# Optimization experiments

Hardware: AMD Instinct MI355X
Metric: run time of the kernel (lower is better)

## Reference

```python
import jax, jax.numpy as jnp
from jax import lax
import numpy as np

D_MODEL = 1024
N_HEADS = 16
D_STATE = D_MODEL // N_HEADS  # 64
EPS = 1e-6


def setup_inputs() -> dict:
    key = jax.random.key(0)
    ks = jax.random.split(key, 8)
    B, S = 4, 4096
    s = 1.0 / np.sqrt(D_MODEL)
    return {
        "x": jax.random.normal(ks[0], (B, S, D_MODEL), dtype=jnp.float32),
        "state": jnp.zeros((B, N_HEADS, D_STATE), dtype=jnp.float32),
        "norm_w": jnp.ones((D_MODEL,), dtype=jnp.float32),
        "Wp": jax.random.normal(ks[1], (D_MODEL, 3 * N_HEADS * D_STATE), dtype=jnp.float32) * s,
        "bp": jax.random.normal(ks[2], (3 * N_HEADS * D_STATE,), dtype=jnp.float32) * 0.01,
        "Wg": jax.random.normal(ks[3], (D_MODEL, D_MODEL), dtype=jnp.float32) * s,
        "bg": jax.random.normal(ks[4], (D_MODEL,), dtype=jnp.float32) * 0.01,
        "Wo": jax.random.normal(ks[5], (D_MODEL, D_MODEL), dtype=jnp.float32) * s,
        "bo": jax.random.normal(ks[6], (D_MODEL,), dtype=jnp.float32) * 0.01,
    }


def reference(x, state, norm_w, Wp, bp, Wg, bg, Wo, bo):
    B, S, D = x.shape
    # RMSNorm
    rms = jnp.sqrt(jnp.mean(x * x, axis=-1, keepdims=True) + EPS)
    xn = norm_w * x / rms
    # input-dependent gate and SSM parameters (all per-timestep, vectorized)
    gate = jax.nn.sigmoid(xn @ Wg + bg)                        # (B,S,D)
    p = (xn @ Wp + bp).reshape(B, S, N_HEADS, 3, D_STATE)
    delta = jax.nn.sigmoid(p[..., 0, :])                       # (B,S,H,Ds)
    Bt = p[..., 1, :]
    Ct = p[..., 2, :]
    # sequential recurrence h_{t+1} = delta_t * h_t + B_t via lax.scan over time
    def step(h, db):
        d, b = db
        h = d * h + b
        return h, h
    dT = jnp.moveaxis(delta, 1, 0)  # (S,B,H,Ds)
    bT = jnp.moveaxis(Bt, 1, 0)
    new_state, hs = lax.scan(step, state, (dT, bT))
    hs = jnp.moveaxis(hs, 0, 1)     # (B,S,H,Ds)
    ssm = (Ct * hs).reshape(B, S, D)
    mixed = gate * ssm + (1.0 - gate) * xn
    y = mixed @ Wo + bo + x         # out_proj + residual (dropout=0)
    return y, new_state
```

## Files before the change

### kernel.cpp

```cpp
#include <hip/hip_runtime.h>
#include <hip/hip_bf16.h>
#include <cstdint>
#include <cstddef>

#define D_MODEL 1024
#define N_HEADS 16
#define D_STATE 64
#define SEQ 4096
#define BATCH 4
#define M_TOK (BATCH * SEQ)
#define N1 4096
#define CLEN 128
#define NCH (SEQ / CLEN)
#define NCHAN (BATCH * D_MODEL)

typedef __attribute__((ext_vector_type(8))) short bf16x8;
typedef __attribute__((ext_vector_type(4))) float f32x4;

__device__ __forceinline__ float sigmoidf_(float x) {
    return 1.0f / (1.0f + __expf(-x));
}

__device__ __forceinline__ void async_load16(const void* g, void* l) {
    __builtin_amdgcn_global_load_lds(
        (__attribute__((address_space(1))) void*)(g),
        (__attribute__((address_space(3))) void*)(l), 16, 0, 0);
}

__global__ __launch_bounds__(256) void transpose_cvt(
    const float* __restrict__ src, __hip_bfloat16* __restrict__ dst,
    int K, int N)
{
    __shared__ float tile[32][33];
    int n0 = blockIdx.x * 32, k0 = blockIdx.y * 32;
    int tx = threadIdx.x, ty = threadIdx.y;
#pragma unroll
    for (int j = 0; j < 32; j += 8)
        tile[ty + j][tx] = src[(size_t)(k0 + ty + j) * N + n0 + tx];
    __syncthreads();
#pragma unroll
    for (int j = 0; j < 32; j += 8)
        dst[(size_t)(n0 + ty + j) * K + k0 + tx] = __float2bfloat16(tile[tx][ty + j]);
}

__global__ __launch_bounds__(256) void rmsnorm_kernel(
    const float* __restrict__ x, const float* __restrict__ w,
    __hip_bfloat16* __restrict__ xn)
{
    int m = blockIdx.x;
    int tid = threadIdx.x;
    const float4* xr = (const float4*)(x + (size_t)m * D_MODEL);
    float4 v = xr[tid];
    float ss = v.x * v.x + v.y * v.y + v.z * v.z + v.w * v.w;
#pragma unroll
    for (int o = 32; o >= 1; o >>= 1) ss += __shfl_xor(ss, o, 64);
    __shared__ float red[4];
    int wave = tid >> 6, lane = tid & 63;
    if (lane == 0) red[wave] = ss;
    __syncthreads();
    float tot = red[0] + red[1] + red[2] + red[3];
    float scale = rsqrtf(tot * (1.0f / D_MODEL) + 1e-6f);
    const float4* wr = (const float4*)w;
    float4 wv = wr[tid];
    __hip_bfloat16 o4[4];
    o4[0] = __float2bfloat16(wv.x * v.x * scale);
    o4[1] = __float2bfloat16(wv.y * v.y * scale);
    o4[2] = __float2bfloat16(wv.z * v.z * scale);
    o4[3] = __float2bfloat16(wv.w * v.w * scale);
    *(uint64_t*)(xn + (size_t)m * D_MODEL + tid * 4) = *(uint64_t*)o4;
}


__device__ __forceinline__ void stage8(const short*& Ag, const short*& Bg,
                                       short* dbase, int stL, int K)
{
    short* la = dbase;
    short* lb = dbase + 16384;
#pragma unroll
    for (int l = 0; l < 4; ++l) {
        async_load16(Ag + (size_t)(l * 64) * K, la + stL + l * 4096);
        async_load16(Bg + (size_t)(l * 64) * K, lb + stL + l * 4096);
    }
    Ag += 64;
    Bg += 64;
}

template <int MODE>
__global__ __launch_bounds__(512, 2) void gemm256(
    const __hip_bfloat16* __restrict__ A,
    const __hip_bfloat16* __restrict__ Bt,
    const float* __restrict__ bias0,
    const float* __restrict__ bias1,
    void* __restrict__ outp, int N, int K)
{
    extern __shared__ short lds[];
    const int tid = threadIdx.x;
    const int wave = tid >> 6, lane = tid & 63;
    const int fr = lane & 15, fq = lane >> 4;
    const int frx = fr & 7;
    const int wm = (wave >> 2) * 128;
    const int wn = (wave & 3) * 64;

    const int gx = gridDim.x;
    const int nwg = gx * gridDim.y;
    const int orig = blockIdx.y * gx + blockIdx.x;
    const int swz = (orig & 7) * (nwg >> 3) + (orig >> 3);
    const int m0 = (swz / gx) * 256;
    const int n0 = (swz % gx) * 256;

    const int rb = tid >> 3, p8 = tid & 7;
    const int lsl = p8 ^ (rb & 7);
    const short* Ag = (const short*)A + (size_t)(m0 + rb) * K + lsl * 8;
    const short* Bg = (const short*)Bt + (size_t)(n0 + rb) * K + lsl * 8;
    const int stL = rb * 64 + p8 * 8;

    const int NT = K >> 6;

    f32x4 acc[2][4][4];
#pragma unroll
    for (int h = 0; h < 2; ++h)
#pragma unroll
        for (int i = 0; i < 4; ++i)
#pragma unroll
            for (int j = 0; j < 4; ++j)
                acc[h][i][j] = (f32x4){0.f, 0.f, 0.f, 0.f};

    stage8(Ag, Bg, lds, stL, K);
    stage8(Ag, Bg, lds + 32768, stL, K);

#define LDA(h, i, kk) (*(const bf16x8*)&Ab[(wm + (h)*64 + (i)*16 + fr) * 64 + \
                                           (((kk)*4 + fq) ^ frx) * 8])
#define LDB(j, kk)    (*(const bf16x8*)&Bb[(wn + (j)*16 + fr) * 64 + \
                                           (((kk)*4 + fq) ^ frx) * 8])

    for (int kt = 0; kt < NT; ++kt) {
        if (kt + 1 < NT) { asm volatile("s_waitcnt vmcnt(8)" ::: "memory"); }
        else             { asm volatile("s_waitcnt vmcnt(0)" ::: "memory"); }
        __builtin_amdgcn_s_barrier();
        __builtin_amdgcn_sched_barrier(0);

        const short* Ab = lds + ((kt & 1) ? 32768 : 0);
        const short* Bb = Ab + 16384;

        bf16x8 af[4][2], b0[2][2], b1[2][2];

#pragma unroll
        for (int i = 0; i < 4; ++i) { af[i][0] = LDA(0, i, 0); af[i][1] = LDA(0, i, 1); }
#pragma unroll
        for (int j = 0; j < 2; ++j) { b0[j][0] = LDB(j, 0); b0[j][1] = LDB(j, 1); }
        __builtin_amdgcn_s_setprio(1);
#pragma unroll
        for (int i = 0; i < 4; ++i)
#pragma unroll
            for (int j = 0; j < 2; ++j) {
                acc[0][i][j] = __builtin_amdgcn_mfma_f32_16x16x32_bf16(af[i][0], b0[j][0], acc[0][i][j], 0, 0, 0);
                acc[0][i][j] = __builtin_amdgcn_mfma_f32_16x16x32_bf16(af[i][1], b0[j][1], acc[0][i][j], 0, 0, 0);
            }
        __builtin_amdgcn_s_setprio(0);
        __builtin_amdgcn_sched_barrier(0);

#pragma unroll
        for (int j = 0; j < 2; ++j) { b1[j][0] = LDB(2 + j, 0); b1[j][1] = LDB(2 + j, 1); }
        __builtin_amdgcn_s_setprio(1);
#pragma unroll
        for (int i = 0; i < 4; ++i)
#pragma unroll
            for (int j = 0; j < 2; ++j) {
                acc[0][i][2 + j] = __builtin_amdgcn_mfma_f32_16x16x32_bf16(af[i][0], b1[j][0], acc[0][i][2 + j], 0, 0, 0);
                acc[0][i][2 + j] = __builtin_amdgcn_mfma_f32_16x16x32_bf16(af[i][1], b1[j][1], acc[0][i][2 + j], 0, 0, 0);
            }
        __builtin_amdgcn_s_setprio(0);
        __builtin_amdgcn_sched_barrier(0);

#pragma unroll
        for (int i = 0; i < 4; ++i) { af[i][0] = LDA(1, i, 0); af[i][1] = LDA(1, i, 1); }
        __builtin_amdgcn_s_setprio(1);
#pragma unroll
        for (int i = 0; i < 4; ++i)
#pragma unroll
            for (int j = 0; j < 2; ++j) {
                acc[1][i][j] = __builtin_amdgcn_mfma_f32_16x16x32_bf16(af[i][0], b0[j][0], acc[1][i][j], 0, 0, 0);
                acc[1][i][j] = __builtin_amdgcn_mfma_f32_16x16x32_bf16(af[i][1], b0[j][1], acc[1][i][j], 0, 0, 0);
            }
        __builtin_amdgcn_s_setprio(0);
        __builtin_amdgcn_sched_barrier(0);

        __builtin_amdgcn_s_setprio(1);
#pragma unroll
        for (int i = 0; i < 4; ++i)
#pragma unroll
            for (int j = 0; j < 2; ++j) {
                acc[1][i][2 + j] = __builtin_amdgcn_mfma_f32_16x16x32_bf16(af[i][0], b1[j][0], acc[1][i][2 + j], 0, 0, 0);
                acc[1][i][2 + j] = __builtin_amdgcn_mfma_f32_16x16x32_bf16(af[i][1], b1[j][1], acc[1][i][2 + j], 0, 0, 0);
            }
        __builtin_amdgcn_s_setprio(0);

        __builtin_amdgcn_sched_barrier(0);
        __builtin_amdgcn_s_barrier();
        if (kt + 2 < NT) stage8(Ag, Bg, lds + ((kt & 1) ? 32768 : 0), stL, K);
    }
#undef LDA
#undef LDB

    if constexpr (MODE == 0) {
        __hip_bfloat16* O = (__hip_bfloat16*)outp;
        float bv[4];
#pragma unroll
        for (int j = 0; j < 4; ++j) {
            int gcol = n0 + wn + j * 16 + fr;
            bv[j] = (gcol < D_MODEL) ? bias0[gcol] : bias1[gcol - D_MODEL];
        }
#pragma unroll
        for (int h = 0; h < 2; ++h)
#pragma unroll
            for (int i = 0; i < 4; ++i)
#pragma unroll
                for (int r = 0; r < 4; ++r) {
                    int grow = m0 + wm + h * 64 + i * 16 + fq * 4 + r;
                    __hip_bfloat16* orow = O + (size_t)grow * N + n0 + wn + fr;
#pragma unroll
                    for (int j = 0; j < 4; ++j)
                        orow[j * 16] = __float2bfloat16(acc[h][i][j][r] + bv[j]);
                }
    } else {
        float* O = (float*)outp;
#pragma unroll
        for (int h = 0; h < 2; ++h)
#pragma unroll
            for (int i = 0; i < 4; ++i)
#pragma unroll
                for (int r = 0; r < 4; ++r) {
                    int grow = m0 + wm + h * 64 + i * 16 + fq * 4 + r;
#pragma unroll
                    for (int j = 0; j < 4; ++j) {
                        int gcol = n0 + wn + j * 16 + fr;
                        O[(size_t)grow * N + gcol] =
                            acc[h][i][j][r] + bias0[gcol] + bias1[(size_t)grow * D_MODEL + gcol];
                    }
                }
    }
}

__global__ __launch_bounds__(256) void scan_part1(
    const __hip_bfloat16* __restrict__ out1,
    float* __restrict__ Abuf, float* __restrict__ Bbuf)
{
    int g = blockIdx.x * 256 + threadIdx.x;
    int chan = g & (NCHAN - 1);
    int c = g >> 12;
    int b = chan >> 10;
    int hd = chan & 1023;
    int h = hd >> 6, d = hd & 63;
    size_t tok0 = (size_t)b * SEQ + (size_t)c * CLEN;
    const __hip_bfloat16* pd = out1 + tok0 * N1 + D_MODEL + h * 192 + d;
    float a = 1.0f, hloc = 0.0f;
#pragma unroll 4
    for (int s = 0; s < CLEN; s++) {
        float dp = __bfloat162float(pd[0]);
        float bt = __bfloat162float(pd[64]);
        float sd = sigmoidf_(dp);
        a *= sd;
        hloc = sd * hloc + bt;
        pd += N1;
    }
    Abuf[c * NCHAN + chan] = a;
    Bbuf[c * NCHAN + chan] = hloc;
}

__global__ __launch_bounds__(256) void scan_comb(
    const float* __restrict__ Abuf, const float* __restrict__ Bbuf,
    const float* __restrict__ state, float* __restrict__ Pbuf,
    float* __restrict__ new_state)
{
    int chan = blockIdx.x * 256 + threadIdx.x;
    float hp = state[chan];
#pragma unroll
    for (int c = 0; c < NCH; c++) {
        Pbuf[c * NCHAN + chan] = hp;
        hp = Abuf[c * NCHAN + chan] * hp + Bbuf[c * NCHAN + chan];
    }
    new_state[chan] = hp;
}

__global__ __launch_bounds__(256) void scan_apply(
    const __hip_bfloat16* __restrict__ out1,
    const __hip_bfloat16* __restrict__ xn,
    const float* __restrict__ Pbuf,
    __hip_bfloat16* __restrict__ mixed)
{
    int g = blockIdx.x * 256 + threadIdx.x;
    int chan = g & (NCHAN - 1);
    int c = g >> 12;
    int b = chan >> 10;
    int hd = chan & 1023;
    int h = hd >> 6, d = hd & 63;
    size_t tok0 = (size_t)b * SEQ + (size_t)c * CLEN;
    const __hip_bfloat16* rbase = out1 + tok0 * N1;
    const __hip_bfloat16* xbase = xn + tok0 * D_MODEL + hd;
    __hip_bfloat16* mbase = mixed + tok0 * D_MODEL + hd;
    const int pcol = D_MODEL + h * 192 + d;
    float hh = Pbuf[c * NCHAN + chan];
#pragma unroll 4
    for (int s = 0; s < CLEN; s++) {
        const __hip_bfloat16* r = rbase + (size_t)s * N1;
        float dp = __bfloat162float(r[pcol]);
        float bt = __bfloat162float(r[pcol + 64]);
        float ct = __bfloat162float(r[pcol + 128]);
        float gp = __bfloat162float(r[hd]);
        float sd = sigmoidf_(dp);
        hh = sd * hh + bt;
        float gg = sigmoidf_(gp);
        float xv = __bfloat162float(xbase[(size_t)s * D_MODEL]);
        mbase[(size_t)s * D_MODEL] = __float2bfloat16(gg * (ct * hh) + (1.0f - gg) * xv);
    }
}

extern "C" void kernel_launch(void* const* d_in, const int* in_sizes, int n_in,
                              void* d_out, int out_size, void* d_ws, size_t ws_size,
                              hipStream_t stream) {
    const float* x      = (const float*)d_in[0];
    const float* state  = (const float*)d_in[1];
    const float* norm_w = (const float*)d_in[2];
    const float* Wp     = (const float*)d_in[3];
    const float* bp     = (const float*)d_in[4];
    const float* Wg     = (const float*)d_in[5];
    const float* bg     = (const float*)d_in[6];
    const float* Wo     = (const float*)d_in[7];
    const float* bo     = (const float*)d_in[8];
    float* out = (float*)d_out;

    __hip_bfloat16* W1T   = (__hip_bfloat16*)d_ws;
    __hip_bfloat16* WoT   = W1T + (size_t)N1 * D_MODEL;
    __hip_bfloat16* xnb   = WoT + (size_t)D_MODEL * D_MODEL;
    __hip_bfloat16* out1  = xnb + (size_t)M_TOK * D_MODEL;
    __hip_bfloat16* mixed = out1 + (size_t)M_TOK * N1;
    float* Abuf = (float*)(mixed + (size_t)M_TOK * D_MODEL);
    float* Bbuf = Abuf + (size_t)NCHAN * NCH;
    float* Pbuf = Bbuf + (size_t)NCHAN * NCH;

    static bool attr_set = false;
    if (!attr_set) {
        hipFuncSetAttribute(reinterpret_cast<const void*>(&gemm256<0>),
                            hipFuncAttributeMaxDynamicSharedMemorySize, 131072);
        hipFuncSetAttribute(reinterpret_cast<const void*>(&gemm256<1>),
                            hipFuncAttributeMaxDynamicSharedMemorySize, 131072);
        attr_set = true;
    }

    dim3 tb(32, 8);
    transpose_cvt<<<dim3(1024 / 32, 1024 / 32), tb, 0, stream>>>(Wg, W1T, 1024, 1024);
    transpose_cvt<<<dim3(3072 / 32, 1024 / 32), tb, 0, stream>>>(
        Wp, W1T + (size_t)D_MODEL * D_MODEL, 1024, 3072);
    transpose_cvt<<<dim3(1024 / 32, 1024 / 32), tb, 0, stream>>>(Wo, WoT, 1024, 1024);

    rmsnorm_kernel<<<M_TOK, 256, 0, stream>>>(x, norm_w, xnb);

    gemm256<0><<<dim3(N1 / 256, M_TOK / 256), 512, 131072, stream>>>(
        xnb, W1T, bg, bp, (void*)out1, N1, D_MODEL);

    scan_part1<<<(NCHAN * NCH) / 256, 256, 0, stream>>>(out1, Abuf, Bbuf);
    scan_comb<<<NCHAN / 256, 256, 0, stream>>>(
        Abuf, Bbuf, state, Pbuf, out + (size_t)M_TOK * D_MODEL);
    scan_apply<<<(NCHAN * NCH) / 256, 256, 0, stream>>>(out1, xnb, Pbuf, mixed);

    gemm256<1><<<dim3(D_MODEL / 256, M_TOK / 256), 512, 131072, stream>>>(
        mixed, WoT, bo, x, (void*)out, D_MODEL, D_MODEL);
}
```

Measured before the change: 391.4 us.

## Interleave next-tile async loads across MFMA phases in bf16 GEMM

Replaces the two-tiles-ahead whole-tile prefetch with a one-tile-ahead scheme. The global-to-LDS loads for the next K tile are split into pairs, each issued between the MFMA sub-phases, with finer vmcnt waits. The first tile's A chunks are loaded in the order the first compute phase needs them, so compute can start before the whole tile lands. The goal is to spread memory traffic across compute and shorten the prologue. In exchange it adds many more workgroup barriers per iteration and a shallower prefetch distance.

```diff
diff --git a/kernel.cpp b/kernel.cpp
--- a/kernel.cpp
+++ b/kernel.cpp
@@ -71,20 +71,6 @@
 }
 
 
-__device__ __forceinline__ void stage8(const short*& Ag, const short*& Bg,
-                                       short* dbase, int stL, int K)
-{
-    short* la = dbase;
-    short* lb = dbase + 16384;
-#pragma unroll
-    for (int l = 0; l < 4; ++l) {
-        async_load16(Ag + (size_t)(l * 64) * K, la + stL + l * 4096);
-        async_load16(Bg + (size_t)(l * 64) * K, lb + stL + l * 4096);
-    }
-    Ag += 64;
-    Bg += 64;
-}
-
 template <int MODE>
 __global__ __launch_bounds__(512, 2) void gemm256(
     const __hip_bfloat16* __restrict__ A,
@@ -110,8 +96,8 @@
 
     const int rb = tid >> 3, p8 = tid & 7;
     const int lsl = p8 ^ (rb & 7);
-    const short* Ag = (const short*)A + (size_t)(m0 + rb) * K + lsl * 8;
-    const short* Bg = (const short*)Bt + (size_t)(n0 + rb) * K + lsl * 8;
+    const short* Ag0 = (const short*)A + (size_t)(m0 + rb) * K + lsl * 8;
+    const short* Bg0 = (const short*)Bt + (size_t)(n0 + rb) * K + lsl * 8;
     const int stL = rb * 64 + p8 * 8;
 
     const int NT = K >> 6;
@@ -125,22 +111,37 @@
             for (int j = 0; j < 4; ++j)
                 acc[h][i][j] = (f32x4){0.f, 0.f, 0.f, 0.f};
 
-    stage8(Ag, Bg, lds, stL, K);
-    stage8(Ag, Bg, lds + 32768, stL, K);
+    {
+        short* la = lds;
+        short* lb = lds + 16384;
+        async_load16(Bg0 + (size_t)(0 * 64) * K, lb + stL + 0 * 4096);
+        async_load16(Bg0 + (size_t)(1 * 64) * K, lb + stL + 1 * 4096);
+        async_load16(Bg0 + (size_t)(2 * 64) * K, lb + stL + 2 * 4096);
+        async_load16(Bg0 + (size_t)(3 * 64) * K, lb + stL + 3 * 4096);
+        async_load16(Ag0 + (size_t)(0 * 64) * K, la + stL + 0 * 4096);
+        async_load16(Ag0 + (size_t)(2 * 64) * K, la + stL + 2 * 4096);
+        async_load16(Ag0 + (size_t)(1 * 64) * K, la + stL + 1 * 4096);
+        async_load16(Ag0 + (size_t)(3 * 64) * K, la + stL + 3 * 4096);
+    }
+    asm volatile("s_waitcnt vmcnt(2)" ::: "memory");
+    __builtin_amdgcn_s_barrier();
+    __builtin_amdgcn_sched_barrier(0);
 
 #define LDA(h, i, kk) (*(const bf16x8*)&Ab[(wm + (h)*64 + (i)*16 + fr) * 64 + \
                                            (((kk)*4 + fq) ^ frx) * 8])
 #define LDB(j, kk)    (*(const bf16x8*)&Bb[(wn + (j)*16 + fr) * 64 + \
                                            (((kk)*4 + fq) ^ frx) * 8])
-
-    for (int kt = 0; kt < NT; ++kt) {
-        if (kt + 1 < NT) { asm volatile("s_waitcnt vmcnt(8)" ::: "memory"); }
-        else             { asm volatile("s_waitcnt vmcnt(0)" ::: "memory"); }
-        __builtin_amdgcn_s_barrier();
-        __builtin_amdgcn_sched_barrier(0);
-
-        const short* Ab = lds + ((kt & 1) ? 32768 : 0);
+#define STAGE_A(c) async_load16(AgN + (size_t)((c) * 64) * K, laN + stL + (c) * 4096)
+#define STAGE_B(c) async_load16(BgN + (size_t)((c) * 64) * K, lbN + stL + (c) * 4096)
+
+    for (int t = 0; t < NT; ++t) {
+        const short* Ab = lds + ((t & 1) ? 32768 : 0);
         const short* Bb = Ab + 16384;
+        short* laN = lds + ((t & 1) ? 0 : 32768);
+        short* lbN = laN + 16384;
+        const short* AgN = Ag0 + (size_t)(t + 1) * 64;
+        const short* BgN = Bg0 + (size_t)(t + 1) * 64;
+        const bool pf = (t + 1 < NT);
 
         bf16x8 af[4][2], b0[2][2], b1[2][2];
 
@@ -148,6 +149,9 @@
         for (int i = 0; i < 4; ++i) { af[i][0] = LDA(0, i, 0); af[i][1] = LDA(0, i, 1); }
 #pragma unroll
         for (int j = 0; j < 2; ++j) { b0[j][0] = LDB(j, 0); b0[j][1] = LDB(j, 1); }
+        if (pf) { STAGE_B(0); STAGE_B(1); }
+        __builtin_amdgcn_s_barrier();
+        __builtin_amdgcn_sched_barrier(0);
         __builtin_amdgcn_s_setprio(1);
 #pragma unroll
         for (int i = 0; i < 4; ++i)
@@ -158,9 +162,14 @@
             }
         __builtin_amdgcn_s_setprio(0);
         __builtin_amdgcn_sched_barrier(0);
+        __builtin_amdgcn_s_barrier();
+        __builtin_amdgcn_sched_barrier(0);
 
 #pragma unroll
         for (int j = 0; j < 2; ++j) { b1[j][0] = LDB(2 + j, 0); b1[j][1] = LDB(2 + j, 1); }
+        if (pf) { STAGE_B(2); STAGE_B(3); }
+        __builtin_amdgcn_s_barrier();
+        __builtin_amdgcn_sched_barrier(0);
         __builtin_amdgcn_s_setprio(1);
 #pragma unroll
         for (int i = 0; i < 4; ++i)
@@ -171,9 +180,16 @@
             }
         __builtin_amdgcn_s_setprio(0);
         __builtin_amdgcn_sched_barrier(0);
+        if (pf) { asm volatile("s_waitcnt vmcnt(4)" ::: "memory"); }
+        else    { asm volatile("s_waitcnt vmcnt(0)" ::: "memory"); }
+        __builtin_amdgcn_s_barrier();
+        __builtin_amdgcn_sched_barrier(0);
 
 #pragma unroll
         for (int i = 0; i < 4; ++i) { af[i][0] = LDA(1, i, 0); af[i][1] = LDA(1, i, 1); }
+        if (pf) { STAGE_A(0); STAGE_A(2); }
+        __builtin_amdgcn_s_barrier();
+        __builtin_amdgcn_sched_barrier(0);
         __builtin_amdgcn_s_setprio(1);
 #pragma unroll
         for (int i = 0; i < 4; ++i)
@@ -184,7 +200,15 @@
             }
         __builtin_amdgcn_s_setprio(0);
         __builtin_amdgcn_sched_barrier(0);
-
+        __builtin_amdgcn_s_barrier();
+        __builtin_amdgcn_sched_barrier(0);
+
+        if (pf) {
+            STAGE_A(1); STAGE_A(3);
+            asm volatile("s_waitcnt vmcnt(2)" ::: "memory");
+        }
+        __builtin_amdgcn_s_barrier();
+        __builtin_amdgcn_sched_barrier(0);
         __builtin_amdgcn_s_setprio(1);
 #pragma unroll
         for (int i = 0; i < 4; ++i)
@@ -194,13 +218,14 @@
                 acc[1][i][2 + j] = __builtin_amdgcn_mfma_f32_16x16x32_bf16(af[i][1], b1[j][1], acc[1][i][2 + j], 0, 0, 0);
             }
         __builtin_amdgcn_s_setprio(0);
-
-        __builtin_amdgcn_sched_barrier(0);
-        __builtin_amdgcn_s_barrier();
-        if (kt + 2 < NT) stage8(Ag, Bg, lds + ((kt & 1) ? 32768 : 0), stL, K);
+        __builtin_amdgcn_sched_barrier(0);
+        __builtin_amdgcn_s_barrier();
+        __builtin_amdgcn_sched_barrier(0);
     }
 #undef LDA
 #undef LDB
+#undef STAGE_A
+#undef STAGE_B
 
     if constexpr (MODE == 0) {
         __hip_bfloat16* O = (__hip_bfloat16*)outp;
```

Measured after the change: 394.1 us. About the same (+0.7%).
